# Kernel optimization log

Hardware: AMD Instinct MI355X
Metric: run time of the kernel (lower is better)

## Reference

```python
import jax, jax.numpy as jnp
import numpy as np

# Gemma3-style config (matches init_kwargs)
NUM_HEADS = 8
NUM_KV_GROUPS = 4
HEAD_DIM = 256
GROUP_SIZE = NUM_HEADS // NUM_KV_GROUPS
SLIDING_WINDOW = 1024
QUERY_PRE_ATTN_SCALAR = 256.0
SCALE = QUERY_PRE_ATTN_SCALAR ** (-0.5)
EPS = 1e-6


def rmsnorm(x, scale):
    # Gemma-style RMSNorm: fp32 variance, zero-centered weight with (1 + scale)
    xf = x.astype(jnp.float32)
    var = jnp.mean(xf * xf, axis=-1, keepdims=True)
    out = xf * jax.lax.rsqrt(var + EPS) * (1.0 + scale.astype(jnp.float32))
    return out.astype(x.dtype)


def sliding_causal_mask(q_len, kv_len, dtype):
    # additive mask [q_len, kv_len]: 0 allowed, -inf blocked
    q_pos = jnp.arange(kv_len - q_len, kv_len)[:, None]
    k_pos = jnp.arange(kv_len)[None, :]
    allowed = (k_pos <= q_pos) & (k_pos >= q_pos - SLIDING_WINDOW + 1)
    return jnp.where(allowed, jnp.zeros((), dtype), jnp.array(-jnp.inf, dtype))


def setup_inputs() -> dict:
    key = jax.random.key(0)
    ks = jax.random.split(key, 5)
    B, T, D = 2, 2048, 2560
    H, G, Hd = NUM_HEADS, NUM_KV_GROUPS, HEAD_DIM
    x = jax.random.normal(ks[0], (B, T, D), dtype=jnp.float32)
    Wq = jax.random.normal(ks[1], (D, H * Hd), dtype=jnp.float32) * 0.02
    Wk = jax.random.normal(ks[2], (D, G * Hd), dtype=jnp.float32) * 0.02
    Wv = jax.random.normal(ks[3], (D, G * Hd), dtype=jnp.float32) * 0.02
    Wo = jax.random.normal(ks[4], (H * Hd, D), dtype=jnp.float32) * 0.02
    q_scale = jnp.zeros((Hd,), dtype=jnp.float32)
    k_scale = jnp.zeros((Hd,), dtype=jnp.float32)
    return {"x": x, "Wq": Wq, "Wk": Wk, "Wv": Wv, "Wo": Wo,
            "q_scale": q_scale, "k_scale": k_scale}


def reference(x, Wq, Wk, Wv, Wo, q_scale, k_scale):
    B, T, D = x.shape
    H, G, g, Hd = NUM_HEADS, NUM_KV_GROUPS, GROUP_SIZE, HEAD_DIM
    # projections
    q = (x @ Wq).reshape(B, T, H, Hd).transpose(0, 2, 1, 3)   # [B,H,T,Hd]
    k = (x @ Wk).reshape(B, T, G, Hd).transpose(0, 2, 1, 3)   # [B,G,T,Hd]
    v = (x @ Wv).reshape(B, T, G, Hd).transpose(0, 2, 1, 3)   # [B,G,T,Hd]
    # qk-norm
    q = rmsnorm(q, q_scale)
    k = rmsnorm(k, k_scale)
    S = T  # no past_kv (prefill)
    # faithful reproduction of the module's head-group reshapes
    q = q.reshape(B, G, g, T, Hd).reshape(B * g, G, T, Hd)
    k = jnp.broadcast_to(k[:, None], (B, g, G, S, Hd)).reshape(B * g, G, S, Hd)
    v = jnp.broadcast_to(v[:, None], (B, g, G, S, Hd)).reshape(B * g, G, S, Hd)
    mask = sliding_causal_mask(T, S, q.dtype)  # [T,S]
    scores = jnp.einsum('bgtd,bgsd->bgts', q, k) * SCALE + mask
    attn = jax.nn.softmax(scores, axis=-1)
    out = jnp.einsum('bgts,bgsd->bgtd', attn, v)
    # faithful inverse reshapes (note g/G order swap vs input, as in source)
    out = out.reshape(B, g, G, T, Hd).reshape(B, H, T, Hd)
    out = out.transpose(0, 2, 1, 3).reshape(B, T, H * Hd)
    return out @ Wo
```

## Files before the change

### kernel.cpp

```cpp
#include <hip/hip_runtime.h>
#include <hip/hip_bf16.h>

typedef unsigned short u16;

#define T_SEQ 2048
#define NTOK 4096
#define D_MODEL 2560
#define NQKV 4096
#define WIN 1024
#define ATTN_SCALE 0.0625f
#define SMAX 17.0f
#define KROW 264

typedef __attribute__((ext_vector_type(8))) short bf16x8;
typedef __attribute__((ext_vector_type(8))) unsigned short u16x8;
typedef __attribute__((ext_vector_type(4))) float f32x4;

__device__ __forceinline__ float bf2f(u16 u) {
  union { unsigned int i; float f; } c; c.i = ((unsigned int)u) << 16; return c.f;
}
__device__ __forceinline__ u16 f2bf(float f) {
  __hip_bfloat16 h = __float2bfloat16(f);
  return __builtin_bit_cast(u16, h);
}
__device__ __forceinline__ u16x8 load8f(const float* p) {
  float4 a = *(const float4*)p;
  float4 b = *(const float4*)(p + 4);
  u16x8 r;
  r[0] = f2bf(a.x); r[1] = f2bf(a.y); r[2] = f2bf(a.z); r[3] = f2bf(a.w);
  r[4] = f2bf(b.x); r[5] = f2bf(b.y); r[6] = f2bf(b.z); r[7] = f2bf(b.w);
  return r;
}
__device__ __forceinline__ void gload_lds16(const u16* g, u16* l) {
  __builtin_amdgcn_global_load_lds(
      (const __attribute__((address_space(1))) void*)g,
      (__attribute__((address_space(3))) void*)l, 16, 0, 0);
}

__global__ __launch_bounds__(256) void cvt_f32_bf16(
    const float* __restrict__ in, u16* __restrict__ out) {
  size_t i = ((size_t)blockIdx.x * 256 + threadIdx.x) * 8;
  *(u16x8*)(out + i) = load8f(in + i);
}

__global__ __launch_bounds__(256) void transpose_w(
    const float* __restrict__ in, u16* __restrict__ out, int K, int N) {
  __shared__ u16 tile[64][65];
  int kb = blockIdx.y * 64, nb = blockIdx.x * 64;
  int t = threadIdx.x;
  int c4 = (t & 15) * 4;
  int r0 = t >> 4;
#pragma unroll
  for (int i = 0; i < 4; ++i) {
    int r = r0 + i * 16;
    float4 v = *(const float4*)(in + (size_t)(kb + r) * N + nb + c4);
    tile[r][c4] = f2bf(v.x); tile[r][c4 + 1] = f2bf(v.y);
    tile[r][c4 + 2] = f2bf(v.z); tile[r][c4 + 3] = f2bf(v.w);
  }
  __syncthreads();
#pragma unroll
  for (int i = 0; i < 4; ++i) {
    int n = r0 + i * 16;
    ushort4 v;
    v.x = tile[c4 + 0][n];
    v.y = tile[c4 + 1][n];
    v.z = tile[c4 + 2][n];
    v.w = tile[c4 + 3][n];
    *(ushort4*)(out + (size_t)(nb + n) * K + kb + c4) = v;
  }
}

__global__ __launch_bounds__(256) void v_transpose(
    const u16* __restrict__ qkv, u16* __restrict__ Vt) {
  int bg = blockIdx.z; int b = bg >> 2, g = bg & 3;
  __shared__ u16 tile[64][65];
  int tb = blockIdx.y * 64, db = blockIdx.x * 64;
  const u16* in = qkv + (size_t)(b * T_SEQ) * NQKV + 3072 + g * 256;
  u16* out = Vt + (size_t)bg * 256 * T_SEQ;
  int t = threadIdx.x;
  int c4 = (t & 15) * 4;
  int r0 = t >> 4;
#pragma unroll
  for (int i = 0; i < 4; ++i) {
    int r = r0 + i * 16;
    ushort4 v = *(const ushort4*)(in + (size_t)(tb + r) * NQKV + db + c4);
    tile[r][c4] = v.x; tile[r][c4 + 1] = v.y; tile[r][c4 + 2] = v.z; tile[r][c4 + 3] = v.w;
  }
  __syncthreads();
#pragma unroll
  for (int i = 0; i < 4; ++i) {
    int n = r0 + i * 16;
    ushort4 v;
    v.x = tile[c4 + 0][n];
    v.y = tile[c4 + 1][n];
    v.z = tile[c4 + 2][n];
    v.w = tile[c4 + 3][n];
    *(ushort4*)(out + (size_t)(db + n) * T_SEQ + tb + c4) = v;
  }
}

template <int WC>
__global__ __launch_bounds__(512, 2) void gemm_256(
    const u16* __restrict__ A, int lda, const u16* __restrict__ Bt, int ldb,
    void* __restrict__ C, int ldc, int K) {
  extern __shared__ ulong2 LDSraw[];
  u16* SA = (u16*)LDSraw;
  u16* SB = SA + 32768;
  const int tid = threadIdx.x;
  const int wave = tid >> 6, lane = tid & 63;
  const int quad = lane >> 4, l16 = lane & 15;
  const int gx = gridDim.x;
  const int orig = blockIdx.y * gx + blockIdx.x;
  const int cpx = (gx * gridDim.y) >> 3;
  const int swz = (orig & 7) * cpx + (orig >> 3);
  const int mblk = (swz / gx) * 256, nblk = (swz % gx) * 256;
  const int wm = (wave >> 2) * 128, wn = (wave & 3) * 64;

  const u16* srcA[2]; const u16* srcB[2];
  int ldsOff[2];
#pragma unroll
  for (int i = 0; i < 2; ++i) {
    int u = i * 512 + tid;
    int hi3 = (u & 7) ^ ((u >> 3) & 7);
    int r = ((u >> 3) << 1) | (hi3 >> 2);
    int cbe = (hi3 & 3) << 3;
    srcA[i] = A + (size_t)(mblk + r) * lda + cbe;
    srcB[i] = Bt + (size_t)(nblk + r) * ldb + cbe;
    ldsOff[i] = (u >> 6) << 9;
  }
  const int unit = ((((l16 & 1) << 2) | quad) ^ ((l16 >> 1) & 7)) << 3;
  const int base_a = ((wm >> 1) + (l16 >> 1)) * 64 + unit;
  const int base_b = ((wn >> 1) + (l16 >> 1)) * 64 + unit;
  const int NK = K >> 5;
  f32x4 acc[8][4] = {};

  auto stage = [&](int s, int i) {
    int slot = s & 3;
    gload_lds16(srcA[i] + s * 32, SA + slot * 8192 + ldsOff[i]);
    gload_lds16(srcB[i] + s * 32, SB + slot * 8192 + ldsOff[i]);
  };

  stage(0, 0); stage(0, 1); stage(1, 0); stage(1, 1); stage(2, 0); stage(2, 1);
  asm volatile("s_waitcnt vmcnt(8)" ::: "memory");
  __builtin_amdgcn_s_barrier();
  asm volatile("" ::: "memory");

  for (int s = 0; s < NK; ++s) {
    const u16* sa = SA + (s & 3) * 8192;
    const u16* sb = SB + (s & 3) * 8192;
    bf16x8 aF[4], bF[4];
#pragma unroll
    for (int t = 0; t < 4; ++t) aF[t] = *(const bf16x8*)(sa + base_a + t * 512);
#pragma unroll
    for (int t = 0; t < 4; ++t) bF[t] = *(const bf16x8*)(sb + base_b + t * 512);
    if (s + 3 < NK) stage(s + 3, 0);
    asm volatile("" ::: "memory");
    __builtin_amdgcn_s_barrier();
    asm volatile("s_waitcnt lgkmcnt(0)" ::: "memory");
    __builtin_amdgcn_sched_barrier(0);
    __builtin_amdgcn_s_setprio(1);
#pragma unroll
    for (int n = 0; n < 4; ++n)
#pragma unroll
      for (int m = 0; m < 4; ++m)
        acc[m][n] = __builtin_amdgcn_mfma_f32_16x16x32_bf16(aF[m], bF[n], acc[m][n], 0, 0, 0);
    __builtin_amdgcn_s_setprio(0);
    asm volatile("" ::: "memory");
    __builtin_amdgcn_s_barrier();
    asm volatile("" ::: "memory");
#pragma unroll
    for (int t = 0; t < 4; ++t) aF[t] = *(const bf16x8*)(sa + base_a + (t + 4) * 512);
    if (s + 3 < NK) stage(s + 3, 1);
    asm volatile("" ::: "memory");
    __builtin_amdgcn_s_barrier();
    asm volatile("s_waitcnt lgkmcnt(0)" ::: "memory");
    __builtin_amdgcn_sched_barrier(0);
    __builtin_amdgcn_s_setprio(1);
#pragma unroll
    for (int n = 0; n < 4; ++n)
#pragma unroll
      for (int m = 0; m < 4; ++m)
        acc[m + 4][n] = __builtin_amdgcn_mfma_f32_16x16x32_bf16(aF[m], bF[n], acc[m + 4][n], 0, 0, 0);
    __builtin_amdgcn_s_setprio(0);
    if (s < NK - 3)       asm volatile("s_waitcnt vmcnt(6)" ::: "memory");
    else if (s == NK - 3) asm volatile("s_waitcnt vmcnt(4)" ::: "memory");
    else if (s == NK - 2) asm volatile("s_waitcnt vmcnt(0)" ::: "memory");
    if (s + 1 < NK) {
      asm volatile("" ::: "memory");
      __builtin_amdgcn_s_barrier();
      asm volatile("" ::: "memory");
    }
  }
#pragma unroll
  for (int m = 0; m < 8; ++m)
#pragma unroll
    for (int n = 0; n < 4; ++n)
#pragma unroll
      for (int r = 0; r < 4; ++r) {
        int row = mblk + wm + m * 16 + quad * 4 + r;
        int col = nblk + wn + n * 16 + l16;
        if constexpr (WC)
          ((float*)C)[(size_t)row * ldc + col] = acc[m][n][r];
        else
          ((u16*)C)[(size_t)row * ldc + col] = f2bf(acc[m][n][r]);
      }
}

template <int WC>
__global__ __launch_bounds__(256, 2) void gemm_fast(
    const u16* __restrict__ A, int lda, const u16* __restrict__ Bt, int ldb,
    void* __restrict__ C, int ldc, int K) {
  __shared__ __align__(16) u16 As[128 * 32];
  __shared__ __align__(16) u16 Bs[128 * 32];
  const int tid = threadIdx.x;
  const int wave = tid >> 6, lane = tid & 63;
  const int quad = lane >> 4, l16 = lane & 15;
  const int mblk = blockIdx.y * 128, nblk = blockIdx.x * 128;
  const int wm = (wave >> 1) * 64, wn = (wave & 1) * 64;
  f32x4 acc[4][4] = {};
  const int c0 = wave * 2;
  for (int k0 = 0; k0 < K; k0 += 32) {
#pragma unroll
    for (int i = 0; i < 2; ++i) {
      int c = c0 + i;
      int flat = c * 64 + lane;
      int row = flat >> 2;
      int kb = (flat & 3) * 8;
      gload_lds16(A + (size_t)(mblk + row) * lda + k0 + kb, As + c * 512);
      gload_lds16(Bt + (size_t)(nblk + row) * ldb + k0 + kb, Bs + c * 512);
    }
    __syncthreads();
    bf16x8 aF[4], bF[4];
#pragma unroll
    for (int t = 0; t < 4; ++t) {
      aF[t] = *(const bf16x8*)(As + (wm + t * 16 + l16) * 32 + quad * 8);
      bF[t] = *(const bf16x8*)(Bs + (wn + t * 16 + l16) * 32 + quad * 8);
    }
#pragma unroll
    for (int tm = 0; tm < 4; ++tm)
#pragma unroll
      for (int tn = 0; tn < 4; ++tn)
        acc[tm][tn] = __builtin_amdgcn_mfma_f32_16x16x32_bf16(aF[tm], bF[tn], acc[tm][tn], 0, 0, 0);
    __syncthreads();
  }
#pragma unroll
  for (int tm = 0; tm < 4; ++tm)
#pragma unroll
    for (int tn = 0; tn < 4; ++tn)
#pragma unroll
      for (int r = 0; r < 4; ++r) {
        int row = mblk + wm + tm * 16 + quad * 4 + r;
        int col = nblk + wn + tn * 16 + l16;
        if constexpr (WC)
          ((float*)C)[(size_t)row * ldc + col] = acc[tm][tn][r];
        else
          ((u16*)C)[(size_t)row * ldc + col] = f2bf(acc[tm][tn][r]);
      }
}

__global__ __launch_bounds__(256, 2) void gemm_f32a(
    const float* __restrict__ A, int lda, const u16* __restrict__ Bt, int ldb,
    u16* __restrict__ C, int ldc, int K) {
  __shared__ __align__(16) u16 As[128 * 32];
  __shared__ __align__(16) u16 Bs[128 * 32];
  const int tid = threadIdx.x;
  const int wave = tid >> 6, lane = tid & 63;
  const int quad = lane >> 4, l16 = lane & 15;
  const int mblk = blockIdx.y * 128, nblk = blockIdx.x * 128;
  const int wm = (wave >> 1) * 64, wn = (wave & 1) * 64;
  f32x4 acc[4][4] = {};
  for (int k0 = 0; k0 < K; k0 += 32) {
#pragma unroll
    for (int i = 0; i < 2; ++i) {
      int u = i * 256 + tid;
      int row = u >> 2;
      int kb = (u & 3) * 8;
      *(u16x8*)(As + row * 32 + kb) = load8f(A + (size_t)(mblk + row) * lda + k0 + kb);
      *(u16x8*)(Bs + row * 32 + kb) = *(const u16x8*)(Bt + (size_t)(nblk + row) * ldb + k0 + kb);
    }
    __syncthreads();
    bf16x8 aF[4], bF[4];
#pragma unroll
    for (int t = 0; t < 4; ++t) {
      aF[t] = *(const bf16x8*)(As + (wm + t * 16 + l16) * 32 + quad * 8);
      bF[t] = *(const bf16x8*)(Bs + (wn + t * 16 + l16) * 32 + quad * 8);
    }
#pragma unroll
    for (int tm = 0; tm < 4; ++tm)
#pragma unroll
      for (int tn = 0; tn < 4; ++tn)
        acc[tm][tn] = __builtin_amdgcn_mfma_f32_16x16x32_bf16(aF[tm], bF[tn], acc[tm][tn], 0, 0, 0);
    __syncthreads();
  }
#pragma unroll
  for (int tm = 0; tm < 4; ++tm)
#pragma unroll
    for (int tn = 0; tn < 4; ++tn)
#pragma unroll
      for (int r = 0; r < 4; ++r) {
        int row = mblk + wm + tm * 16 + quad * 4 + r;
        int col = nblk + wn + tn * 16 + l16;
        C[(size_t)row * ldc + col] = f2bf(acc[tm][tn][r]);
      }
}

__global__ __launch_bounds__(256) void rmsnorm_qk(
    u16* __restrict__ qkv, const float* __restrict__ q_scale,
    const float* __restrict__ k_scale) {
  int wv = blockIdx.x * 4 + (threadIdx.x >> 6);
  int lane = threadIdx.x & 63;
  int token = wv / 12, j = wv - token * 12;
  const float* sc = (j < 8) ? q_scale : k_scale;
  int col = (j < 8) ? j * 256 : 2048 + (j - 8) * 256;
  u16* p = qkv + (size_t)token * NQKV + col;
  int d = lane * 4;
  ushort4 raw = *(const ushort4*)(p + d);
  float x0 = bf2f(raw.x), x1 = bf2f(raw.y), x2 = bf2f(raw.z), x3 = bf2f(raw.w);
  float sum = x0 * x0 + x1 * x1 + x2 * x2 + x3 * x3;
#pragma unroll
  for (int m = 1; m < 64; m <<= 1) sum += __shfl_xor(sum, m, 64);
  float r = rsqrtf(sum * (1.0f / 256.0f) + 1e-6f);
  float4 sv = *(const float4*)(sc + d);
  ushort4 o;
  o.x = f2bf(x0 * r * (1.0f + sv.x));
  o.y = f2bf(x1 * r * (1.0f + sv.y));
  o.z = f2bf(x2 * r * (1.0f + sv.z));
  o.w = f2bf(x3 * r * (1.0f + sv.w));
  *(ushort4*)(p + d) = o;
}

__global__ __launch_bounds__(256) void attn_fused(
    u16* __restrict__ qkv, const u16* __restrict__ Vt) {
  const int qt = blockIdx.x, h = blockIdx.y, b = blockIdx.z;
  const int g = h & 3;
  const int tid = threadIdx.x;
  const int wave = tid >> 6, lane = tid & 63;
  const int quad = lane >> 4, l16 = lane & 15;
  const int t0 = qt * 64;
  const int tw = t0 + wave * 16;
  __shared__ __align__(16) u16 Ks[32 * KROW];
  __shared__ __align__(16) u16 Vs[256 * 32];
  __shared__ __align__(16) u16 Ps[4][16 * 32];
  bf16x8 qF[8];
  {
    const u16* qrow = qkv + (size_t)(b * T_SEQ + tw + l16) * NQKV + h * 256;
#pragma unroll
    for (int kc = 0; kc < 8; ++kc)
      qF[kc] = *(const bf16x8*)(qrow + kc * 32 + quad * 8);
  }
  const u16* vt_base = Vt + (size_t)(b * 4 + g) * 256 * T_SEQ;
  f32x4 o[16] = {};
  float lsum[4] = {0.f, 0.f, 0.f, 0.f};
  int s_lo = t0 - (WIN - 1); if (s_lo < 0) s_lo = 0; s_lo &= ~31;
  const int s_hi = t0 + 63;
  for (int sb = s_lo; sb <= s_hi; sb += 32) {
#pragma unroll
    for (int i = 0; i < 4; ++i) {
      int u = i * 256 + tid;
      int krow = u >> 5, kcb = u & 31;
      *(u16x8*)(Ks + krow * KROW + kcb * 8) =
          *(const u16x8*)(qkv + (size_t)(b * T_SEQ + sb + krow) * NQKV + 2048 + g * 256 + kcb * 8);
      int dim = u >> 2, kvp = (u & 3) * 8;
      *(u16x8*)(Vs + dim * 32 + kvp) =
          *(const u16x8*)(vt_base + (size_t)dim * T_SEQ + sb + kvp);
    }
    __syncthreads();
    f32x4 st[2] = {};
#pragma unroll
    for (int nt = 0; nt < 2; ++nt)
#pragma unroll
      for (int kc = 0; kc < 8; ++kc) {
        bf16x8 kF = *(const bf16x8*)(Ks + (nt * 16 + l16) * KROW + kc * 32 + quad * 8);
        st[nt] = __builtin_amdgcn_mfma_f32_16x16x32_bf16(qF[kc], kF, st[nt], 0, 0, 0);
      }
    const bool full = (sb + 31 <= tw) && (sb >= tw + 15 - (WIN - 1));
#pragma unroll
    for (int r = 0; r < 4; ++r) {
      float v0 = st[0][r] * ATTN_SCALE - SMAX;
      float v1 = st[1][r] * ATTN_SCALE - SMAX;
      if (!full) {
        int t = tw + quad * 4 + r;
        int c0s = sb + l16, c1s = c0s + 16;
        v0 = (c0s <= t && c0s > t - WIN) ? v0 : -3.0e38f;
        v1 = (c1s <= t && c1s > t - WIN) ? v1 : -3.0e38f;
      }
      float p0 = __expf(v0);
      float p1 = __expf(v1);
      Ps[wave][(quad * 4 + r) * 32 + l16] = f2bf(p0);
      Ps[wave][(quad * 4 + r) * 32 + 16 + l16] = f2bf(p1);
      lsum[r] += p0 + p1;
    }
    __syncthreads();
    bf16x8 pF = *(const bf16x8*)(&Ps[wave][l16 * 32 + quad * 8]);
#pragma unroll
    for (int nt = 0; nt < 16; ++nt) {
      bf16x8 vF = *(const bf16x8*)(Vs + (nt * 16 + l16) * 32 + quad * 8);
      o[nt] = __builtin_amdgcn_mfma_f32_16x16x32_bf16(pF, vF, o[nt], 0, 0, 0);
    }
    __syncthreads();
  }
#pragma unroll
  for (int r = 0; r < 4; ++r) {
    float s = lsum[r];
    s += __shfl_xor(s, 1, 64);
    s += __shfl_xor(s, 2, 64);
    s += __shfl_xor(s, 4, 64);
    s += __shfl_xor(s, 8, 64);
    lsum[r] = s;
  }
#pragma unroll
  for (int r = 0; r < 4; ++r) {
    float inv = 1.0f / lsum[r];
    int t = tw + quad * 4 + r;
    u16* orow = qkv + (size_t)(b * T_SEQ + t) * NQKV + h * 256;
#pragma unroll
    for (int nt = 0; nt < 16; ++nt)
      orow[nt * 16 + l16] = f2bf(o[nt][r] * inv);
  }
}

extern "C" void kernel_launch(void* const* d_in, const int* in_sizes, int n_in,
                              void* d_out, int out_size, void* d_ws, size_t ws_size,
                              hipStream_t stream) {
  const float* x       = (const float*)d_in[0];
  const float* Wq      = (const float*)d_in[1];
  const float* Wk      = (const float*)d_in[2];
  const float* Wv      = (const float*)d_in[3];
  const float* Wo      = (const float*)d_in[4];
  const float* q_scale = (const float*)d_in[5];
  const float* k_scale = (const float*)d_in[6];

  u16* qkv = (u16*)d_ws;
  const size_t BIG_WS = (size_t)NTOK * NQKV * 2
                      + (size_t)NTOK * D_MODEL * 2
                      + (size_t)NQKV * D_MODEL * 2;

  if (ws_size >= BIG_WS) {
    (void)hipFuncSetAttribute(reinterpret_cast<const void*>(&gemm_256<0>),
                              hipFuncAttributeMaxDynamicSharedMemorySize, 131072);
    (void)hipFuncSetAttribute(reinterpret_cast<const void*>(&gemm_256<1>),
                              hipFuncAttributeMaxDynamicSharedMemorySize, 131072);
    u16* xbf = qkv + (size_t)NTOK * NQKV;
    u16* WT  = xbf + (size_t)NTOK * D_MODEL;
    cvt_f32_bf16<<<dim3(NTOK * D_MODEL / (256 * 8)), 256, 0, stream>>>(x, xbf);
    transpose_w<<<dim3(32, 40), 256, 0, stream>>>(Wq, WT, D_MODEL, 2048);
    transpose_w<<<dim3(16, 40), 256, 0, stream>>>(Wk, WT + (size_t)2048 * D_MODEL, D_MODEL, 1024);
    transpose_w<<<dim3(16, 40), 256, 0, stream>>>(Wv, WT + (size_t)3072 * D_MODEL, D_MODEL, 1024);
    gemm_256<0><<<dim3(16, 16), 512, 131072, stream>>>(xbf, D_MODEL, WT, D_MODEL, qkv, NQKV, D_MODEL);
    rmsnorm_qk<<<dim3(12288), 256, 0, stream>>>(qkv, q_scale, k_scale);
    v_transpose<<<dim3(4, 32, 8), 256, 0, stream>>>(qkv, xbf);
    attn_fused<<<dim3(T_SEQ / 64, 8, 2), 256, 0, stream>>>(qkv, xbf);
    transpose_w<<<dim3(40, 32), 256, 0, stream>>>(Wo, WT, 2048, D_MODEL);
    gemm_256<1><<<dim3(10, 16), 512, 131072, stream>>>(qkv, NQKV, WT, 2048, d_out, D_MODEL, 2048);
  } else {
    u16* WT = qkv + (size_t)NTOK * NQKV;
    transpose_w<<<dim3(32, 40), 256, 0, stream>>>(Wq, WT, D_MODEL, 2048);
    gemm_f32a<<<dim3(16, 32), 256, 0, stream>>>(x, D_MODEL, WT, D_MODEL, qkv, NQKV, D_MODEL);
    transpose_w<<<dim3(16, 40), 256, 0, stream>>>(Wk, WT, D_MODEL, 1024);
    gemm_f32a<<<dim3(8, 32), 256, 0, stream>>>(x, D_MODEL, WT, D_MODEL, qkv + 2048, NQKV, D_MODEL);
    transpose_w<<<dim3(16, 40), 256, 0, stream>>>(Wv, WT, D_MODEL, 1024);
    gemm_f32a<<<dim3(8, 32), 256, 0, stream>>>(x, D_MODEL, WT, D_MODEL, qkv + 3072, NQKV, D_MODEL);
    rmsnorm_qk<<<dim3(12288), 256, 0, stream>>>(qkv, q_scale, k_scale);
    v_transpose<<<dim3(4, 32, 8), 256, 0, stream>>>(qkv, WT);
    attn_fused<<<dim3(T_SEQ / 64, 8, 2), 256, 0, stream>>>(qkv, WT);
    transpose_w<<<dim3(40, 32), 256, 0, stream>>>(Wo, WT, 2048, D_MODEL);
    gemm_fast<1><<<dim3(20, 32), 256, 0, stream>>>(qkv, NQKV, WT, 2048, d_out, D_MODEL, 2048);
  }
}
```

Before: 385.2 us.

## Double-buffer attention K/V tiles and use gemm_fast for output projection

Attention now prefetches the next K/V tile into registers while computing on the current one. Writes go to a second LDS buffer, which removes one of the two barriers per tile. The V and P LDS rows are padded to 40 elements to reduce bank conflicts. The output projection switches from the 256-tile gemm with 131 KB dynamic LDS to gemm_fast with a 256-thread grid. The extra buffers raise LDS use and register pressure, which may lower occupancy.

```diff
diff --git a/kernel.cpp b/kernel.cpp
--- a/kernel.cpp
+++ b/kernel.cpp
@@ -11,6 +11,7 @@
 #define ATTN_SCALE 0.0625f
 #define SMAX 17.0f
 #define KROW 264
+#define VROW 40
 
 typedef __attribute__((ext_vector_type(8))) short bf16x8;
 typedef __attribute__((ext_vector_type(8))) unsigned short u16x8;
@@ -338,9 +339,9 @@
   const int quad = lane >> 4, l16 = lane & 15;
   const int t0 = qt * 64;
   const int tw = t0 + wave * 16;
-  __shared__ __align__(16) u16 Ks[32 * KROW];
-  __shared__ __align__(16) u16 Vs[256 * 32];
-  __shared__ __align__(16) u16 Ps[4][16 * 32];
+  __shared__ __align__(16) u16 Ks[2][32 * KROW];
+  __shared__ __align__(16) u16 Vs[2][256 * VROW];
+  __shared__ __align__(16) u16 Ps[4][16 * VROW];
   bf16x8 qF[8];
   {
     const u16* qrow = qkv + (size_t)(b * T_SEQ + tw + l16) * NQKV + h * 256;
@@ -349,28 +350,51 @@
       qF[kc] = *(const bf16x8*)(qrow + kc * 32 + quad * 8);
   }
   const u16* vt_base = Vt + (size_t)(b * 4 + g) * 256 * T_SEQ;
+  const u16* k_base = qkv + (size_t)(b * T_SEQ) * NQKV + 2048 + g * 256;
   f32x4 o[16] = {};
   float lsum[4] = {0.f, 0.f, 0.f, 0.f};
   int s_lo = t0 - (WIN - 1); if (s_lo < 0) s_lo = 0; s_lo &= ~31;
   const int s_hi = t0 + 63;
-  for (int sb = s_lo; sb <= s_hi; sb += 32) {
-#pragma unroll
-    for (int i = 0; i < 4; ++i) {
-      int u = i * 256 + tid;
-      int krow = u >> 5, kcb = u & 31;
-      *(u16x8*)(Ks + krow * KROW + kcb * 8) =
-          *(const u16x8*)(qkv + (size_t)(b * T_SEQ + sb + krow) * NQKV + 2048 + g * 256 + kcb * 8);
-      int dim = u >> 2, kvp = (u & 3) * 8;
-      *(u16x8*)(Vs + dim * 32 + kvp) =
-          *(const u16x8*)(vt_base + (size_t)dim * T_SEQ + sb + kvp);
-    }
-    __syncthreads();
+  const int n_tiles = (s_hi - s_lo + 32) >> 5;
+
+  u16x8 rK[4], rV[4];
+#define ISSUE_LOADS(sb)                                                       \
+  {                                                                           \
+    _Pragma("unroll")                                                         \
+    for (int i = 0; i < 4; ++i) {                                             \
+      int u = i * 256 + tid;                                                  \
+      int krow = u >> 5, kcb = u & 31;                                        \
+      rK[i] = *(const u16x8*)(k_base + (size_t)((sb) + krow) * NQKV + kcb * 8);\
+      int dim = u >> 2, kvp = (u & 3) * 8;                                    \
+      rV[i] = *(const u16x8*)(vt_base + (size_t)dim * T_SEQ + (sb) + kvp);    \
+    }                                                                         \
+  }
+#define WRITE_LDS(buf)                                                        \
+  {                                                                           \
+    _Pragma("unroll")                                                         \
+    for (int i = 0; i < 4; ++i) {                                             \
+      int u = i * 256 + tid;                                                  \
+      int krow = u >> 5, kcb = u & 31;                                        \
+      *(u16x8*)(Ks[buf] + krow * KROW + kcb * 8) = rK[i];                     \
+      int dim = u >> 2, kvp = (u & 3) * 8;                                    \
+      *(u16x8*)(Vs[buf] + dim * VROW + kvp) = rV[i];                          \
+    }                                                                         \
+  }
+
+  ISSUE_LOADS(s_lo);
+  WRITE_LDS(0);
+  __syncthreads();
+
+  for (int ti = 0; ti < n_tiles; ++ti) {
+    const int sb = s_lo + ti * 32;
+    const int buf = ti & 1;
+    if (ti + 1 < n_tiles) ISSUE_LOADS(sb + 32);
     f32x4 st[2] = {};
 #pragma unroll
     for (int nt = 0; nt < 2; ++nt)
 #pragma unroll
       for (int kc = 0; kc < 8; ++kc) {
-        bf16x8 kF = *(const bf16x8*)(Ks + (nt * 16 + l16) * KROW + kc * 32 + quad * 8);
+        bf16x8 kF = *(const bf16x8*)(Ks[buf] + (nt * 16 + l16) * KROW + kc * 32 + quad * 8);
         st[nt] = __builtin_amdgcn_mfma_f32_16x16x32_bf16(qF[kc], kF, st[nt], 0, 0, 0);
       }
     const bool full = (sb + 31 <= tw) && (sb >= tw + 15 - (WIN - 1));
@@ -386,19 +410,21 @@
       }
       float p0 = __expf(v0);
       float p1 = __expf(v1);
-      Ps[wave][(quad * 4 + r) * 32 + l16] = f2bf(p0);
-      Ps[wave][(quad * 4 + r) * 32 + 16 + l16] = f2bf(p1);
+      Ps[wave][(quad * 4 + r) * VROW + l16] = f2bf(p0);
+      Ps[wave][(quad * 4 + r) * VROW + 16 + l16] = f2bf(p1);
       lsum[r] += p0 + p1;
     }
+    bf16x8 pF = *(const bf16x8*)(&Ps[wave][l16 * VROW + quad * 8]);
+#pragma unroll
+    for (int nt = 0; nt < 16; ++nt) {
+      bf16x8 vF = *(const bf16x8*)(Vs[buf] + (nt * 16 + l16) * VROW + quad * 8);
+      o[nt] = __builtin_amdgcn_mfma_f32_16x16x32_bf16(pF, vF, o[nt], 0, 0, 0);
+    }
+    if (ti + 1 < n_tiles) WRITE_LDS(buf ^ 1);
     __syncthreads();
-    bf16x8 pF = *(const bf16x8*)(&Ps[wave][l16 * 32 + quad * 8]);
-#pragma unroll
-    for (int nt = 0; nt < 16; ++nt) {
-      bf16x8 vF = *(const bf16x8*)(Vs + (nt * 16 + l16) * 32 + quad * 8);
-      o[nt] = __builtin_amdgcn_mfma_f32_16x16x32_bf16(pF, vF, o[nt], 0, 0, 0);
-    }
-    __syncthreads();
-  }
+  }
+#undef ISSUE_LOADS
+#undef WRITE_LDS
 #pragma unroll
   for (int r = 0; r < 4; ++r) {
     float s = lsum[r];
@@ -437,8 +463,6 @@
 
   if (ws_size >= BIG_WS) {
     (void)hipFuncSetAttribute(reinterpret_cast<const void*>(&gemm_256<0>),
-                              hipFuncAttributeMaxDynamicSharedMemorySize, 131072);
-    (void)hipFuncSetAttribute(reinterpret_cast<const void*>(&gemm_256<1>),
                               hipFuncAttributeMaxDynamicSharedMemorySize, 131072);
     u16* xbf = qkv + (size_t)NTOK * NQKV;
     u16* WT  = xbf + (size_t)NTOK * D_MODEL;
@@ -451,7 +475,7 @@
     v_transpose<<<dim3(4, 32, 8), 256, 0, stream>>>(qkv, xbf);
     attn_fused<<<dim3(T_SEQ / 64, 8, 2), 256, 0, stream>>>(qkv, xbf);
     transpose_w<<<dim3(40, 32), 256, 0, stream>>>(Wo, WT, 2048, D_MODEL);
-    gemm_256<1><<<dim3(10, 16), 512, 131072, stream>>>(qkv, NQKV, WT, 2048, d_out, D_MODEL, 2048);
+    gemm_fast<1><<<dim3(20, 32), 256, 0, stream>>>(qkv, NQKV, WT, 2048, d_out, D_MODEL, 2048);
   } else {
     u16* WT = qkv + (size_t)NTOK * NQKV;
     transpose_w<<<dim3(32, 40), 256, 0, stream>>>(Wq, WT, D_MODEL, 2048);
```

After: 378.6 us. Within noise of the previous version (-1.7%).
